# Optimization experiments

Hardware: AMD Instinct MI355X
Metric: run time of the kernel (lower is better)

Reference implementation:

```python
import jax, jax.numpy as jnp
import numpy as np

PI = float(np.pi)


def _layernorm(x, g, b, eps=1e-5):
    mu = jnp.mean(x, axis=-1, keepdims=True)
    var = jnp.var(x, axis=-1, keepdims=True)
    return (x - mu) * jax.lax.rsqrt(var + eps) * g + b


def setup_inputs() -> dict:
    key = jax.random.key(0)
    B, L, D, P = 4, 2048, 256, 32
    ks = jax.random.split(key, 16)

    def lin_w(k, fi, fo):
        return (jax.random.normal(k, (fi, fo), dtype=jnp.float32) / np.sqrt(fi)).astype(jnp.float32)

    inp = {
        'x': jax.random.normal(ks[0], (B, L, D), dtype=jnp.float32),
        'pos_phases': jax.random.normal(ks[1], (L, P), dtype=jnp.float32) * PI,
        'w_mem1v': lin_w(ks[2], D, P), 'b_mem1v': jnp.zeros((P,), jnp.float32),
        'w_mem1o': lin_w(ks[3], P, D), 'b_mem1o': jnp.zeros((D,), jnp.float32),
        'w_off': lin_w(ks[4], D + P, P), 'b_off': jnp.zeros((P,), jnp.float32),
        'w_key': lin_w(ks[5], D, P), 'b_key': jnp.zeros((P,), jnp.float32),
        'w_val': lin_w(ks[6], D, D), 'b_val': jnp.zeros((D,), jnp.float32),
        'w_sk1': lin_w(ks[7], 2 * D, D), 'b_sk1': jnp.zeros((D,), jnp.float32),
        'w_sk2': lin_w(ks[8], D, P), 'b_sk2': jnp.zeros((P,), jnp.float32),
        'w_gate': lin_w(ks[9], D, 1), 'b_gate': jnp.zeros((1,), jnp.float32),
        'ln_g': jnp.ones((D,), jnp.float32), 'ln_b': jnp.zeros((D,), jnp.float32),
        'w_out': lin_w(ks[10], D, D), 'b_out': jnp.zeros((D,), jnp.float32),
    }
    return inp


def reference(x, pos_phases, w_mem1v, b_mem1v, w_mem1o, b_mem1o, w_off, b_off,
              w_key, b_key, w_val, b_val, w_sk1, b_sk1, w_sk2, b_sk2,
              w_gate, b_gate, ln_g, ln_b, w_out, b_out):
    B, L, D = x.shape
    P = pos_phases.shape[-1]

    pos_cos = jnp.cos(pos_phases)  # [L,P]
    pos_sin = jnp.sin(pos_phases)

    # Memory 1: flat [B,L,P] phasor cumulative memory
    v1 = x @ w_mem1v + b_mem1v                       # [B,L,P]
    mem1_cos = jnp.cumsum(pos_cos[None] * v1, axis=1)
    mem1_sin = jnp.cumsum(pos_sin[None] * v1, axis=1)

    offset_input = jnp.concatenate([x, jnp.broadcast_to(pos_phases[None], (B, L, P))], axis=-1)
    offset = jnp.tanh(offset_input @ w_off + b_off) * PI
    oc, os = jnp.cos(offset), jnp.sin(offset)
    query_cos = pos_cos[None] * oc - pos_sin[None] * os
    query_sin = pos_sin[None] * oc + pos_cos[None] * os
    pos_ret = (mem1_cos * query_cos + mem1_sin * query_sin) / np.sqrt(P)
    pos_out = pos_ret @ w_mem1o + b_mem1o            # [B,L,D]

    # Memory 2: full [B,L,P,D] phasor KV cumulative memory
    key_phases = jnp.tanh(x @ w_key + b_key) * PI    # [B,L,P]
    key_cos, key_sin = jnp.cos(key_phases), jnp.sin(key_phases)
    values = x @ w_val + b_val                       # [B,L,D]
    store_gate = jax.nn.sigmoid(x @ w_gate + b_gate) # [B,L,1]

    positions = jnp.arange(1, L + 1, dtype=x.dtype)[None, :, None]
    context_avg = jnp.cumsum(x, axis=1) / positions
    h = jax.nn.gelu(jnp.concatenate([x, context_avg], axis=-1) @ w_sk1 + b_sk1, approximate=False)
    storage_phases = jnp.tanh(h @ w_sk2 + b_sk2) * PI  # [B,L,P]

    gated_v = values * store_gate                    # [B,L,D]
    kv_mem_cos = jnp.cumsum(jnp.cos(storage_phases)[..., None] * gated_v[:, :, None, :], axis=1)  # [B,L,P,D]
    kv_mem_sin = jnp.cumsum(jnp.sin(storage_phases)[..., None] * gated_v[:, :, None, :], axis=1)

    gate_cumsum = jnp.clip(jnp.cumsum(store_gate, axis=1), 1.0, None)  # [B,L,1]
    kv_retrieved = jnp.einsum('blpd,blp->bld', kv_mem_cos, key_cos) + \
                   jnp.einsum('blpd,blp->bld', kv_mem_sin, key_sin)
    kv_retrieved = kv_retrieved / (jnp.sqrt(gate_cumsum) * np.sqrt(P))

    combined = pos_out + kv_retrieved
    return x + _layernorm(combined, ln_g, ln_b) @ w_out + b_out
```

## Files before the change

### kernel.cpp

```cpp
#include <hip/hip_runtime.h>
#include <hip/hip_bf16.h>

constexpr int B_ = 4;
constexpr int L_ = 2048;
constexpr int D_ = 256;
constexpr int P_ = 32;
constexpr int CL = 32;
constexpr int NC = L_ / CL;

#define PI_F 3.14159265358979323846f
#define INV_SQRT_P 0.17677669529663687f

typedef __attribute__((ext_vector_type(8))) short short8_t;
typedef __attribute__((ext_vector_type(4))) float floatx4;

static __device__ inline short f2bf(float f) {
  unsigned int u;
  __builtin_memcpy(&u, &f, 4);
  unsigned int r = (u + 0x7fffu + ((u >> 16) & 1u)) >> 16;
  return (short)r;
}
static __device__ inline float bf2f(short s) {
  unsigned int u = ((unsigned int)(unsigned short)s) << 16;
  float f;
  __builtin_memcpy(&f, &u, 4);
  return f;
}

__global__ void wprep(const float* __restrict__ x, const float* __restrict__ pos,
                      const float* __restrict__ w_val, const float* __restrict__ w_mem1v,
                      const float* __restrict__ w_off, const float* __restrict__ b_off,
                      const float* __restrict__ w_key, const float* __restrict__ w_gate,
                      const float* __restrict__ w_sk1, const float* __restrict__ w_out,
                      const float* __restrict__ w_sk2, const float* __restrict__ w_mem1o,
                      short* __restrict__ WA, short* __restrict__ W1,
                      short* __restrict__ WO, short* __restrict__ W2T,
                      short* __restrict__ W1OT,
                      short* __restrict__ xbf, float* __restrict__ poff,
                      float* __restrict__ ctxsum) {
  int blk = blockIdx.x, tid = threadIdx.x;
  if (blk < 384) {
    int idx = blk * 256 + tid;
    int n = idx >> 8, k = idx & 255;
    float v;
    if (n < 256) v = w_val[k * 256 + n];
    else if (n < 288) v = w_mem1v[k * 32 + (n - 256)];
    else if (n < 320) v = w_off[k * 32 + (n - 288)];
    else if (n < 352) v = w_key[k * 32 + (n - 320)];
    else if (n == 352) v = w_gate[k];
    else v = 0.f;
    WA[idx] = f2bf(v);
  } else if (blk < 896) {
    int idx = (blk - 384) * 256 + tid;
    int n = idx >> 9, k = idx & 511;
    W1[idx] = f2bf(w_sk1[k * 256 + n]);
  } else if (blk < 1152) {
    int idx = (blk - 896) * 256 + tid;
    int n = idx >> 8, k = idx & 255;
    WO[idx] = f2bf(w_out[k * 256 + n]);
  } else if (blk < 1184) {
    int idx = (blk - 1152) * 256 + tid;
    int p = idx >> 8, k = idx & 255;
    W2T[idx] = f2bf(w_sk2[k * 32 + p]);
  } else if (blk < 1216) {
    int idx = (blk - 1184) * 256 + tid;
    int d = idx >> 5, p = idx & 31;
    W1OT[idx] = f2bf(w_mem1o[p * 256 + d]);
  } else if (blk < 3264) {
    int idx = ((blk - 1216) * 256 + tid) * 4;
    float4 v = *(const float4*)&x[idx];
    short4 o;
    o.x = f2bf(v.x); o.y = f2bf(v.y); o.z = f2bf(v.z); o.w = f2bf(v.w);
    *(short4*)&xbf[idx] = o;
  } else if (blk < 3520) {
    int idx = (blk - 3264) * 256 + tid;
    int l = idx >> 5, p = idx & 31;
    float a = b_off[p];
#pragma unroll 8
    for (int j = 0; j < 32; ++j) a += pos[l * 32 + j] * w_off[(256 + j) * 32 + p];
    poff[idx] = a;
  } else {
    int c2 = blk - 3520;
    int b = c2 >> 6, ch = c2 & 63;
    int xb = (b * L_ + ch * 32) * 256 + tid;
    float s = 0.f;
#pragma unroll 8
    for (int i = 0; i < 32; ++i) s += x[xb + i * 256];
    ctxsum[c2 * 256 + tid] = s;
  }
}

__global__ __launch_bounds__(384, 3) void gemmA3(const short* __restrict__ xbf,
                                                 const short* __restrict__ WA,
                                                 const float* __restrict__ pos,
                                                 const float* __restrict__ poff,
                                                 const float* __restrict__ b_mem1v,
                                                 const float* __restrict__ b_key,
                                                 const float* __restrict__ b_gate,
                                                 const float* __restrict__ b_val,
                                                 float* __restrict__ m1cT,
                                                 float* __restrict__ m1sT,
                                                 float* __restrict__ qc,
                                                 float* __restrict__ qs,
                                                 short* __restrict__ K2bf,
                                                 short* __restrict__ gvT,
                                                 float* __restrict__ sg) {
  __shared__ float YL[16][132];
  __shared__ float gsh[16];
  int tid = threadIdx.x;
  int lane = tid & 63, w = tid >> 6;
  int ml = lane & 15, quad = lane >> 4, kq = quad * 8;
  int bc = blockIdx.x;
  int bc32 = bc >> 1, half = bc & 1;
  int tok0 = bc * 16;
  floatx4 acc[4] = {};
  const short* A0p = &xbf[(tok0 + ml) * 256 + kq];
  const short* Bp = &WA[(w * 64 + ml) * 256 + kq];
#pragma unroll
  for (int ks = 0; ks < 8; ++ks) {
    short8_t a0 = *(const short8_t*)(A0p + ks * 32);
#pragma unroll
    for (int nt = 0; nt < 4; ++nt) {
      short8_t b = *(const short8_t*)(Bp + nt * 16 * 256 + ks * 32);
      acc[nt] = __builtin_amdgcn_mfma_f32_16x16x32_bf16(a0, b, acc[nt], 0, 0, 0);
    }
  }
  if (w >= 4) {
#pragma unroll
    for (int nt = 0; nt < 4; ++nt) {
      int col = (w - 4) * 64 + nt * 16 + ml;
#pragma unroll
      for (int r = 0; r < 4; ++r)
        YL[quad * 4 + r][col] = acc[nt][r];
    }
  }
  __syncthreads();
  if (tid < 256) {
#pragma unroll
    for (int it = 0; it < 2; ++it) {
      int idx = it * 256 + tid;
      int t = idx >> 5, p = idx & 31;
      int tok = tok0 + t, l = tok & (L_ - 1);
      int b = tok >> 11;
      float v1 = YL[t][p] + b_mem1v[p];
      float ph = pos[l * 32 + p];
      float pc = cosf(ph), ps = sinf(ph);
      int idxT = (b * 32 + p) * L_ + l;
      m1cT[idxT] = pc * v1;
      m1sT[idxT] = ps * v1;
      float off = tanhf(YL[t][32 + p] + poff[l * 32 + p]) * PI_F;
      float oc = cosf(off), os = sinf(off);
      int gidx = tok * 32 + p;
      qc[gidx] = pc * oc - ps * os;
      qs[gidx] = ps * oc + pc * os;
      float kp = tanhf(YL[t][64 + p] + b_key[p]) * PI_F;
      K2bf[tok * 64 + p] = f2bf(cosf(kp));
      K2bf[tok * 64 + 32 + p] = f2bf(sinf(kp));
      if (p == 0) {
        float g = 1.f / (1.f + expf(-(YL[t][96] + b_gate[0])));
        sg[tok] = g;
        gsh[t] = g;
      }
    }
  }
  __syncthreads();
  if (w < 4) {
#pragma unroll
    for (int nt = 0; nt < 4; ++nt) {
      int d = w * 64 + nt * 16 + ml;
      float bv = b_val[d];
      int t0 = quad * 4;
      short4 o;
      o.x = f2bf((acc[nt][0] + bv) * gsh[t0 + 0]);
      o.y = f2bf((acc[nt][1] + bv) * gsh[t0 + 1]);
      o.z = f2bf((acc[nt][2] + bv) * gsh[t0 + 2]);
      o.w = f2bf((acc[nt][3] + bv) * gsh[t0 + 3]);
      *(short4*)&gvT[(bc32 * 256 + d) * 32 + half * 16 + t0] = o;
    }
  }
}

__global__ void scan_all(float* __restrict__ m1cT, float* __restrict__ m1sT,
                         float* __restrict__ sg, const float* __restrict__ x,
                         const float* __restrict__ ctxsum, short* __restrict__ ctxbf) {
  int blk = blockIdx.x;
  int tid = threadIdx.x;
  if (blk >= 260) {
    int c2 = blk - 260;
    int b = c2 >> 6, ch = c2 & 63;
    float run = 0.f;
    int sb = b * 64 * 256 + tid;
    int c = 0;
    for (; c + 8 <= ch; c += 8) {
      float t0 = ctxsum[sb + (c + 0) * 256];
      float t1 = ctxsum[sb + (c + 1) * 256];
      float t2 = ctxsum[sb + (c + 2) * 256];
      float t3 = ctxsum[sb + (c + 3) * 256];
      float t4 = ctxsum[sb + (c + 4) * 256];
      float t5 = ctxsum[sb + (c + 5) * 256];
      float t6 = ctxsum[sb + (c + 6) * 256];
      float t7 = ctxsum[sb + (c + 7) * 256];
      run += ((t0 + t1) + (t2 + t3)) + ((t4 + t5) + (t6 + t7));
    }
    for (; c < ch; ++c) run += ctxsum[sb + c * 256];
    int xb = (b * L_ + ch * 32) * 256 + tid;
#pragma unroll 8
    for (int i = 0; i < 32; ++i) {
      run += x[xb + i * 256];
      int l = ch * 32 + i;
      ctxbf[xb + i * 256] = f2bf(run / (float)(l + 1));
    }
    return;
  }
  int lane = tid & 63, wid = tid >> 6;
  __shared__ float wsum[4];
  float carry = 0.f;
  float* arr;
  int base;
  if (blk < 256) {
    arr = (blk < 128) ? m1cT : m1sT;
    base = (blk & 127) * L_;
  } else {
    arr = sg;
    base = (blk - 256) * L_;
  }
  float v[8];
#pragma unroll
  for (int i = 0; i < 8; ++i) v[i] = arr[base + i * 256 + tid];
#pragma unroll
  for (int i = 0; i < 8; ++i) {
    float vv = v[i];
#pragma unroll
    for (int off = 1; off < 64; off <<= 1) {
      float n = __shfl_up(vv, off, 64);
      if (lane >= off) vv += n;
    }
    if (lane == 63) wsum[wid] = vv;
    __syncthreads();
    float add = carry;
    for (int w = 0; w < wid; ++w) add += wsum[w];
    arr[base + i * 256 + tid] = vv + add;
    carry += wsum[0] + wsum[1] + wsum[2] + wsum[3];
    __syncthreads();
  }
}

union __align__(16) CDMem {
  short As[32][520];
  struct { short HS[32][280]; short SPL[64][40]; } h;
};
__global__ __launch_bounds__(512, 4) void gemmCD(const short* __restrict__ xbf,
                                                 const short* __restrict__ ctxbf,
                                                 const short* __restrict__ W1,
                                                 const float* __restrict__ b_sk1,
                                                 const short* __restrict__ W2T,
                                                 const float* __restrict__ b_sk2,
                                                 const short* __restrict__ gvT,
                                                 short* __restrict__ SPbf,
                                                 short* __restrict__ UT) {
  __shared__ CDMem sm;
  int tid = threadIdx.x;
  int bc = blockIdx.x;
  int tok0 = bc * 32;
  int lane = tid & 63, w = tid >> 6;
  int ml = lane & 15, quad = lane >> 4, kq = quad * 8;
#pragma unroll
  for (int pass = 0; pass < 4; ++pass) {
    int idx = pass * 512 + tid;
    int row = idx >> 6, c8 = idx & 63;
    int col = c8 * 8;
    const short* src = (col < 256) ? &xbf[(tok0 + row) * 256 + col]
                                   : &ctxbf[(tok0 + row) * 256 + col - 256];
    *(short8_t*)&sm.As[row][col] = *(const short8_t*)src;
  }
  __syncthreads();
  int n0w = w * 32;
  floatx4 acc[2][2] = {};
#pragma unroll
  for (int kt = 0; kt < 16; ++kt) {
    short8_t a0 = *(short8_t*)&sm.As[ml][kt * 32 + kq];
    short8_t a1 = *(short8_t*)&sm.As[16 + ml][kt * 32 + kq];
    short8_t b0 = *(const short8_t*)&W1[(n0w + ml) * 512 + kt * 32 + kq];
    short8_t b1 = *(const short8_t*)&W1[(n0w + 16 + ml) * 512 + kt * 32 + kq];
    acc[0][0] = __builtin_amdgcn_mfma_f32_16x16x32_bf16(a0, b0, acc[0][0], 0, 0, 0);
    acc[0][1] = __builtin_amdgcn_mfma_f32_16x16x32_bf16(a0, b1, acc[0][1], 0, 0, 0);
    acc[1][0] = __builtin_amdgcn_mfma_f32_16x16x32_bf16(a1, b0, acc[1][0], 0, 0, 0);
    acc[1][1] = __builtin_amdgcn_mfma_f32_16x16x32_bf16(a1, b1, acc[1][1], 0, 0, 0);
  }
  short hv[2][2][4];
#pragma unroll
  for (int nt = 0; nt < 2; ++nt) {
    float bv = b_sk1[n0w + nt * 16 + ml];
#pragma unroll
    for (int mt = 0; mt < 2; ++mt)
#pragma unroll
      for (int r = 0; r < 4; ++r) {
        float v = acc[mt][nt][r] + bv;
        float g = 0.5f * v * (1.f + erff(v * 0.70710678118654752f));
        hv[mt][nt][r] = f2bf(g);
      }
  }
  __syncthreads();
#pragma unroll
  for (int mt = 0; mt < 2; ++mt)
#pragma unroll
    for (int nt = 0; nt < 2; ++nt)
#pragma unroll
      for (int r = 0; r < 4; ++r)
        sm.h.HS[mt * 16 + quad * 4 + r][n0w + nt * 16 + ml] = hv[mt][nt][r];
  __syncthreads();
  if (w < 4) {
    int th = w & 1, ph = w >> 1;
    floatx4 pacc = {};
#pragma unroll
    for (int s = 0; s < 8; ++s) {
      short8_t a = *(short8_t*)&sm.h.HS[th * 16 + ml][s * 32 + kq];
      short8_t b0 = *(const short8_t*)&W2T[(ph * 16 + ml) * 256 + s * 32 + kq];
      pacc = __builtin_amdgcn_mfma_f32_16x16x32_bf16(a, b0, pacc, 0, 0, 0);
    }
    int p = ph * 16 + ml;
    float bs = b_sk2[p];
#pragma unroll
    for (int r = 0; r < 4; ++r) {
      int tl = th * 16 + quad * 4 + r;
      int tok = tok0 + tl;
      float sp = tanhf(pacc[r] + bs) * PI_F;
      short c = f2bf(cosf(sp)), s2 = f2bf(sinf(sp));
      sm.h.SPL[p][tl] = c;
      sm.h.SPL[32 + p][tl] = s2;
      SPbf[tok * 64 + p] = c;
      SPbf[tok * 64 + 32 + p] = s2;
    }
  }
  __syncthreads();
  short8_t a[4];
#pragma unroll
  for (int mt = 0; mt < 4; ++mt) a[mt] = *(short8_t*)&sm.h.SPL[mt * 16 + ml][kq];
  floatx4 acc3[4][2] = {};
#pragma unroll
  for (int nt = 0; nt < 2; ++nt) {
    int d = w * 32 + nt * 16 + ml;
    short8_t b = *(const short8_t*)&gvT[(bc * 256 + d) * 32 + kq];
#pragma unroll
    for (int mt = 0; mt < 4; ++mt)
      acc3[mt][nt] = __builtin_amdgcn_mfma_f32_16x16x32_bf16(a[mt], b, acc3[mt][nt], 0, 0, 0);
  }
#pragma unroll
  for (int mt = 0; mt < 4; ++mt)
#pragma unroll
    for (int nt = 0; nt < 2; ++nt) {
      int d = w * 32 + nt * 16 + ml;
      short4 o;
      o.x = f2bf(acc3[mt][nt][0]);
      o.y = f2bf(acc3[mt][nt][1]);
      o.z = f2bf(acc3[mt][nt][2]);
      o.w = f2bf(acc3[mt][nt][3]);
      *(short4*)&UT[(bc * 256 + d) * 64 + mt * 16 + quad * 4] = o;
    }
}

__global__ void kernelE(short* __restrict__ UT) {
  int t = blockIdx.x * 256 + threadIdx.x;
  int pi = t >> 1, half = t & 1;
  int q = pi & 63;
  int d = (pi >> 6) & 255;
  int b = pi >> 14;
  const int cs = 256 * 64;
  int base = ((b * NC) * 256 + d) * 64 + q + half * 32 * cs;
  short v[32];
#pragma unroll
  for (int c = 0; c < 32; ++c) v[c] = UT[base + c * cs];
  float tot = 0.f;
#pragma unroll
  for (int c = 0; c < 32; ++c) tot += bf2f(v[c]);
  float other = __shfl_xor(tot, 1, 64);
  float run = half ? other : 0.f;
#pragma unroll
  for (int c = 0; c < 32; ++c) {
    UT[base + c * cs] = f2bf(run);
    run += bf2f(v[c]);
  }
}

struct __align__(16) FGMem {
  short SL[32][40];
  short PR[32][40];
  float CMB[32][260];
  short CBN[32][280];
  float LG[256], LB[256];
  float scl[32], mu_s[32], rs_s[32];
};
__global__ __launch_bounds__(512, 4) void fgOut(const short* __restrict__ UT,
                                                const short* __restrict__ SPbf,
                                                const short* __restrict__ K2bf,
                                                const short* __restrict__ gvT,
                                                const float* __restrict__ sgc,
                                                const float* __restrict__ m1cT,
                                                const float* __restrict__ m1sT,
                                                const float* __restrict__ qc,
                                                const float* __restrict__ qs,
                                                const short* __restrict__ W1OT,
                                                const float* __restrict__ b_mem1o,
                                                const float* __restrict__ ln_g,
                                                const float* __restrict__ ln_b,
                                                const short* __restrict__ WO,
                                                const float* __restrict__ b_out,
                                                const float* __restrict__ x,
                                                float* __restrict__ out) {
  __shared__ FGMem sm;
  int tid5 = threadIdx.x;
  int bc = blockIdx.x;
  int lbase = bc * CL;
  int bb = bc >> 6, lloc = (bc & 63) * 32;
  if (tid5 < 32) sm.scl[tid5] = rsqrtf(fmaxf(sgc[lbase + tid5], 1.f)) * INV_SQRT_P;
  if (tid5 >= 256 && tid5 < 512) {
    int d = tid5 - 256;
    sm.LG[d] = ln_g[d];
    sm.LB[d] = ln_b[d];
  }
#pragma unroll
  for (int it = 0; it < 2; ++it) {
    int i = it * 512 + tid5;
    int pp = i >> 5, t = i & 31;
    int gT = (bb * 32 + pp) * L_ + lloc + t;
    int g = (lbase + t) * 32 + pp;
    sm.PR[t][pp] = f2bf((m1cT[gT] * qc[g] + m1sT[gT] * qs[g]) * INV_SQRT_P);
  }
  int lane = tid5 & 63, w = tid5 >> 6;
  int ml = lane & 15, quad = lane >> 4, kq = quad * 8;
  int d0 = w * 32;
  floatx4 acc[2][2] = {};
  short8_t ka0 = *(const short8_t*)&K2bf[(lbase + ml) * 64 + kq];
  short8_t ka1 = *(const short8_t*)&K2bf[(lbase + 16 + ml) * 64 + kq];
  short8_t kb0 = *(const short8_t*)&K2bf[(lbase + ml) * 64 + 32 + kq];
  short8_t kb1 = *(const short8_t*)&K2bf[(lbase + 16 + ml) * 64 + 32 + kq];
#pragma unroll
  for (int nt = 0; nt < 2; ++nt) {
    short8_t b = *(const short8_t*)&UT[(bc * 256 + d0 + nt * 16 + ml) * 64 + kq];
    acc[0][nt] = __builtin_amdgcn_mfma_f32_16x16x32_bf16(ka0, b, acc[0][nt], 0, 0, 0);
    acc[1][nt] = __builtin_amdgcn_mfma_f32_16x16x32_bf16(ka1, b, acc[1][nt], 0, 0, 0);
  }
  if (w == 0) {
    floatx4 sacc[2][2] = {};
#pragma unroll
    for (int ks2 = 0; ks2 < 2; ++ks2) {
      short8_t a0 = (ks2 == 0) ? ka0 : kb0;
      short8_t a1 = (ks2 == 0) ? ka1 : kb1;
      short8_t b0 = *(const short8_t*)&SPbf[(lbase + ml) * 64 + ks2 * 32 + kq];
      short8_t b1 = *(const short8_t*)&SPbf[(lbase + 16 + ml) * 64 + ks2 * 32 + kq];
      sacc[0][0] = __builtin_amdgcn_mfma_f32_16x16x32_bf16(a0, b0, sacc[0][0], 0, 0, 0);
      sacc[0][1] = __builtin_amdgcn_mfma_f32_16x16x32_bf16(a0, b1, sacc[0][1], 0, 0, 0);
      sacc[1][0] = __builtin_amdgcn_mfma_f32_16x16x32_bf16(a1, b0, sacc[1][0], 0, 0, 0);
      sacc[1][1] = __builtin_amdgcn_mfma_f32_16x16x32_bf16(a1, b1, sacc[1][1], 0, 0, 0);
    }
#pragma unroll
    for (int mt = 0; mt < 2; ++mt)
#pragma unroll
      for (int nt = 0; nt < 2; ++nt)
#pragma unroll
        for (int r = 0; r < 4; ++r) {
          int trow = mt * 16 + quad * 4 + r;
          int scol = nt * 16 + ml;
          float v = (scol <= trow) ? sacc[mt][nt][r] : 0.f;
          sm.SL[trow][scol] = f2bf(v);
        }
  }
  __syncthreads();
#pragma unroll
  for (int nt = 0; nt < 2; ++nt) {
    short8_t b = *(const short8_t*)&UT[(bc * 256 + d0 + nt * 16 + ml) * 64 + 32 + kq];
    acc[0][nt] = __builtin_amdgcn_mfma_f32_16x16x32_bf16(kb0, b, acc[0][nt], 0, 0, 0);
    acc[1][nt] = __builtin_amdgcn_mfma_f32_16x16x32_bf16(kb1, b, acc[1][nt], 0, 0, 0);
  }
  {
    short8_t a0 = *(short8_t*)&sm.SL[ml][kq];
    short8_t a1 = *(short8_t*)&sm.SL[16 + ml][kq];
#pragma unroll
    for (int nt = 0; nt < 2; ++nt) {
      short8_t b = *(const short8_t*)&gvT[(bc * 256 + d0 + nt * 16 + ml) * 32 + kq];
      acc[0][nt] = __builtin_amdgcn_mfma_f32_16x16x32_bf16(a0, b, acc[0][nt], 0, 0, 0);
      acc[1][nt] = __builtin_amdgcn_mfma_f32_16x16x32_bf16(a1, b, acc[1][nt], 0, 0, 0);
    }
  }
  floatx4 macc[2][2] = {};
  {
    short8_t a0 = *(short8_t*)&sm.PR[ml][kq];
    short8_t a1 = *(short8_t*)&sm.PR[16 + ml][kq];
#pragma unroll
    for (int nt = 0; nt < 2; ++nt) {
      short8_t b = *(const short8_t*)&W1OT[(d0 + nt * 16 + ml) * 32 + kq];
      macc[0][nt] = __builtin_amdgcn_mfma_f32_16x16x32_bf16(a0, b, macc[0][nt], 0, 0, 0);
      macc[1][nt] = __builtin_amdgcn_mfma_f32_16x16x32_bf16(a1, b, macc[1][nt], 0, 0, 0);
    }
  }
#pragma unroll
  for (int mt = 0; mt < 2; ++mt)
#pragma unroll
    for (int nt = 0; nt < 2; ++nt) {
      int d = d0 + nt * 16 + ml;
      float bm = b_mem1o[d];
#pragma unroll
      for (int r = 0; r < 4; ++r) {
        int t = mt * 16 + quad * 4 + r;
        sm.CMB[t][d] = acc[mt][nt][r] * sm.scl[t] + macc[mt][nt][r] + bm;
      }
    }
  __syncthreads();
  {
    int t = tid5 >> 4, g = tid5 & 15;
    float s = 0.f, s2 = 0.f;
#pragma unroll
    for (int j = 0; j < 16; ++j) {
      float v = sm.CMB[t][g + j * 16];
      s += v;
      s2 += v * v;
    }
#pragma unroll
    for (int m = 1; m < 16; m <<= 1) {
      s += __shfl_xor(s, m, 64);
      s2 += __shfl_xor(s2, m, 64);
    }
    if (g == 0) {
      float mu = s / (float)D_;
      float var = s2 / (float)D_ - mu * mu;
      sm.mu_s[t] = mu;
      sm.rs_s[t] = rsqrtf(var + 1e-5f);
    }
  }
  __syncthreads();
#pragma unroll
  for (int it = 0; it < 16; ++it) {
    int i = it * 512 + tid5;
    int t = i >> 8, d = i & 255;
    sm.CBN[t][d] = f2bf((sm.CMB[t][d] - sm.mu_s[t]) * sm.rs_s[t] * sm.LG[d] + sm.LB[d]);
  }
  __syncthreads();
  floatx4 acc2[2][2] = {};
#pragma unroll
  for (int kt = 0; kt < 8; ++kt) {
    short8_t a0 = *(short8_t*)&sm.CBN[ml][kt * 32 + kq];
    short8_t a1 = *(short8_t*)&sm.CBN[16 + ml][kt * 32 + kq];
#pragma unroll
    for (int nt = 0; nt < 2; ++nt) {
      short8_t b = *(const short8_t*)&WO[(d0 + nt * 16 + ml) * 256 + kt * 32 + kq];
      acc2[0][nt] = __builtin_amdgcn_mfma_f32_16x16x32_bf16(a0, b, acc2[0][nt], 0, 0, 0);
      acc2[1][nt] = __builtin_amdgcn_mfma_f32_16x16x32_bf16(a1, b, acc2[1][nt], 0, 0, 0);
    }
  }
#pragma unroll
  for (int nt = 0; nt < 2; ++nt) {
    int n = d0 + nt * 16 + ml;
    float bv = b_out[n];
#pragma unroll
    for (int mt = 0; mt < 2; ++mt)
#pragma unroll
      for (int r = 0; r < 4; ++r) {
        int tok = lbase + mt * 16 + quad * 4 + r;
        out[tok * 256 + n] = x[tok * 256 + n] + acc2[mt][nt][r] + bv;
      }
  }
}

extern "C" void kernel_launch(void* const* d_in, const int* in_sizes, int n_in,
                              void* d_out, int out_size, void* d_ws, size_t ws_size,
                              hipStream_t stream) {
  const float* x = (const float*)d_in[0];
  const float* pos = (const float*)d_in[1];
  const float* w_mem1v = (const float*)d_in[2];
  const float* b_mem1v = (const float*)d_in[3];
  const float* w_mem1o = (const float*)d_in[4];
  const float* b_mem1o = (const float*)d_in[5];
  const float* w_off = (const float*)d_in[6];
  const float* b_off = (const float*)d_in[7];
  const float* w_key = (const float*)d_in[8];
  const float* b_key = (const float*)d_in[9];
  const float* w_val = (const float*)d_in[10];
  const float* b_val = (const float*)d_in[11];
  const float* w_sk1 = (const float*)d_in[12];
  const float* b_sk1 = (const float*)d_in[13];
  const float* w_sk2 = (const float*)d_in[14];
  const float* b_sk2 = (const float*)d_in[15];
  const float* w_gate = (const float*)d_in[16];
  const float* b_gate = (const float*)d_in[17];
  const float* ln_g = (const float*)d_in[18];
  const float* ln_b = (const float*)d_in[19];
  const float* w_out = (const float*)d_in[20];
  const float* b_out = (const float*)d_in[21];
  float* out = (float*)d_out;
  float* ws = (float*)d_ws;

  const int BLP = B_ * L_ * P_;
  const int BLD = B_ * L_ * D_;
  float* m1cT = ws;
  float* m1sT = m1cT + BLP;
  float* qc = m1sT + BLP;
  float* qs = qc + BLP;
  float* sg = qs + BLP;
  float* poff = sg + B_ * L_;
  float* ctxsum = poff + L_ * P_;
  short* UT = (short*)(ctxsum + B_ * 64 * 256);
  short* xbf = UT + (size_t)B_ * NC * 256 * 64;
  short* ctxbf = xbf + BLD;
  short* hs = ctxbf + BLD;
  short* gvT = hs + BLD;
  short* K2bf = gvT + BLD;
  short* SPbf = K2bf + B_ * L_ * 64;
  short* WA = SPbf + B_ * L_ * 64;
  short* W1 = WA + 384 * 256;
  short* WO = W1 + 256 * 512;
  short* W2T = WO + 256 * 256;
  short* W1OT = W2T + 32 * 256;

  wprep<<<3776, 256, 0, stream>>>(x, pos, w_val, w_mem1v, w_off, b_off, w_key, w_gate,
                                  w_sk1, w_out, w_sk2, w_mem1o, WA, W1, WO, W2T, W1OT,
                                  xbf, poff, ctxsum);
  gemmA3<<<512, 384, 0, stream>>>(xbf, WA, pos, poff, b_mem1v, b_key, b_gate, b_val,
                                  m1cT, m1sT, qc, qs, K2bf, gvT, sg);
  scan_all<<<516, 256, 0, stream>>>(m1cT, m1sT, sg, x, ctxsum, ctxbf);
  gemmCD<<<256, 512, 0, stream>>>(xbf, ctxbf, W1, b_sk1, W2T, b_sk2, gvT, SPbf, UT);
  kernelE<<<512, 256, 0, stream>>>(UT);
  fgOut<<<256, 512, 0, stream>>>(UT, SPbf, K2bf, gvT, sg, m1cT, m1sT, qc, qs,
                                 W1OT, b_mem1o, ln_g, ln_b, WO, b_out, x, out);
}
```

Baseline: 172.3 us.

## Fuse context-average computation into gemmCD and merge bf16 cast with chunk sums

Removes the ctxbf intermediate by computing the running context average directly into gemmCD's shared-memory A tile from x and the per-chunk sums. It also merges the x-to-bf16 conversion with the chunk-sum pass in wprep so x is read once there. The scan kernel is restructured so each wave scans a contiguous 512-element segment with a single barrier, and it is moved after kernelE. In fgOut, the PR tile build now runs on waves 1-7 alongside wave 0's MFMA work. Together these cut kernel launches work, global traffic and barriers, at the cost of gemmCD rereading x and recomputing chunk prefixes per block.

```diff
diff --git a/kernel.cpp b/kernel.cpp
--- a/kernel.cpp
+++ b/kernel.cpp
@@ -38,6 +38,7 @@
                       short* __restrict__ W1OT,
                       short* __restrict__ xbf, float* __restrict__ poff,
                       float* __restrict__ ctxsum) {
+  __shared__ float2 psum[2][128];
   int blk = blockIdx.x, tid = threadIdx.x;
   if (blk < 384) {
     int idx = blk * 256 + tid;
@@ -66,27 +67,39 @@
     int idx = (blk - 1184) * 256 + tid;
     int d = idx >> 5, p = idx & 31;
     W1OT[idx] = f2bf(w_mem1o[p * 256 + d]);
-  } else if (blk < 3264) {
-    int idx = ((blk - 1216) * 256 + tid) * 4;
-    float4 v = *(const float4*)&x[idx];
-    short4 o;
-    o.x = f2bf(v.x); o.y = f2bf(v.y); o.z = f2bf(v.z); o.w = f2bf(v.w);
-    *(short4*)&xbf[idx] = o;
-  } else if (blk < 3520) {
-    int idx = (blk - 3264) * 256 + tid;
+  } else if (blk < 1472) {
+    int idx = (blk - 1216) * 256 + tid;
     int l = idx >> 5, p = idx & 31;
     float a = b_off[p];
 #pragma unroll 8
     for (int j = 0; j < 32; ++j) a += pos[l * 32 + j] * w_off[(256 + j) * 32 + p];
     poff[idx] = a;
   } else {
-    int c2 = blk - 3520;
+    int c2 = blk - 1472;
     int b = c2 >> 6, ch = c2 & 63;
-    int xb = (b * L_ + ch * 32) * 256 + tid;
-    float s = 0.f;
-#pragma unroll 8
-    for (int i = 0; i < 32; ++i) s += x[xb + i * 256];
-    ctxsum[c2 * 256 + tid] = s;
+    int d2 = (tid & 127) * 2, h = tid >> 7;
+    int tokb = b * L_ + ch * 32 + h * 16;
+    float2 xv[16];
+#pragma unroll
+    for (int i = 0; i < 16; ++i)
+      xv[i] = *(const float2*)&x[(tokb + i) * 256 + d2];
+    float2 s = {0.f, 0.f};
+#pragma unroll
+    for (int i = 0; i < 16; ++i) { s.x += xv[i].x; s.y += xv[i].y; }
+#pragma unroll
+    for (int i = 0; i < 16; ++i) {
+      short2 o;
+      o.x = f2bf(xv[i].x);
+      o.y = f2bf(xv[i].y);
+      *(short2*)&xbf[(tokb + i) * 256 + d2] = o;
+    }
+    psum[h][tid & 127] = s;
+    __syncthreads();
+    if (h == 0) {
+      float2 o = psum[1][tid & 127];
+      float2 tot = {s.x + o.x, s.y + o.y};
+      *(float2*)&ctxsum[c2 * 256 + d2] = tot;
+    }
   }
 }
 
@@ -181,15 +194,78 @@
 }
 
 __global__ void scan_all(float* __restrict__ m1cT, float* __restrict__ m1sT,
-                         float* __restrict__ sg, const float* __restrict__ x,
-                         const float* __restrict__ ctxsum, short* __restrict__ ctxbf) {
+                         float* __restrict__ sg) {
+  __shared__ float wsum[4];
   int blk = blockIdx.x;
   int tid = threadIdx.x;
-  if (blk >= 260) {
-    int c2 = blk - 260;
-    int b = c2 >> 6, ch = c2 & 63;
-    float run = 0.f;
-    int sb = b * 64 * 256 + tid;
+  int lane = tid & 63, w = tid >> 6;
+  float* arr;
+  int base;
+  if (blk < 256) {
+    arr = (blk < 128) ? m1cT : m1sT;
+    base = (blk & 127) * L_;
+  } else {
+    arr = sg;
+    base = (blk - 256) * L_;
+  }
+  int sbase = base + w * 512;
+  float v[8];
+#pragma unroll
+  for (int i = 0; i < 8; ++i) v[i] = arr[sbase + i * 64 + lane];
+  float carry = 0.f;
+#pragma unroll
+  for (int i = 0; i < 8; ++i) {
+    float vv = v[i];
+#pragma unroll
+    for (int off = 1; off < 64; off <<= 1) {
+      float n = __shfl_up(vv, off, 64);
+      if (lane >= off) vv += n;
+    }
+    vv += carry;
+    v[i] = vv;
+    carry = __shfl(vv, 63, 64);
+  }
+  if (lane == 0) wsum[w] = carry;
+  __syncthreads();
+  float off = 0.f;
+  for (int ww = 0; ww < w; ++ww) off += wsum[ww];
+#pragma unroll
+  for (int i = 0; i < 8; ++i) arr[sbase + i * 64 + lane] = v[i] + off;
+}
+
+union __align__(16) CDMem {
+  short As[32][520];
+  struct { short HS[32][280]; short SPL[64][40]; } h;
+};
+__global__ __launch_bounds__(512, 4) void gemmCD(const short* __restrict__ xbf,
+                                                 const float* __restrict__ x,
+                                                 const float* __restrict__ ctxsum,
+                                                 const short* __restrict__ W1,
+                                                 const float* __restrict__ b_sk1,
+                                                 const short* __restrict__ W2T,
+                                                 const float* __restrict__ b_sk2,
+                                                 const short* __restrict__ gvT,
+                                                 short* __restrict__ SPbf,
+                                                 short* __restrict__ UT) {
+  __shared__ CDMem sm;
+  __shared__ float stmp[256];
+  int tid = threadIdx.x;
+  int bc = blockIdx.x;
+  int tok0 = bc * 32;
+  int bI = bc >> 6, ch = bc & 63;
+  int lane = tid & 63, w = tid >> 6;
+  int ml = lane & 15, quad = lane >> 4, kq = quad * 8;
+#pragma unroll
+  for (int pass = 0; pass < 2; ++pass) {
+    int idx = pass * 512 + tid;
+    int row = idx >> 5, c8 = idx & 31;
+    *(short8_t*)&sm.As[row][c8 * 8] =
+        *(const short8_t*)&xbf[(tok0 + row) * 256 + c8 * 8];
+  }
+  {
+    int d = tid & 255, h = tid >> 8;
+    float cp = 0.f;
+    int sb = bI * 64 * 256 + d;
     int c = 0;
     for (; c + 8 <= ch; c += 8) {
       float t0 = ctxsum[sb + (c + 0) * 256];
@@ -200,78 +276,25 @@
       float t5 = ctxsum[sb + (c + 5) * 256];
       float t6 = ctxsum[sb + (c + 6) * 256];
       float t7 = ctxsum[sb + (c + 7) * 256];
-      run += ((t0 + t1) + (t2 + t3)) + ((t4 + t5) + (t6 + t7));
-    }
-    for (; c < ch; ++c) run += ctxsum[sb + c * 256];
-    int xb = (b * L_ + ch * 32) * 256 + tid;
-#pragma unroll 8
-    for (int i = 0; i < 32; ++i) {
-      run += x[xb + i * 256];
-      int l = ch * 32 + i;
-      ctxbf[xb + i * 256] = f2bf(run / (float)(l + 1));
-    }
-    return;
-  }
-  int lane = tid & 63, wid = tid >> 6;
-  __shared__ float wsum[4];
-  float carry = 0.f;
-  float* arr;
-  int base;
-  if (blk < 256) {
-    arr = (blk < 128) ? m1cT : m1sT;
-    base = (blk & 127) * L_;
-  } else {
-    arr = sg;
-    base = (blk - 256) * L_;
-  }
-  float v[8];
-#pragma unroll
-  for (int i = 0; i < 8; ++i) v[i] = arr[base + i * 256 + tid];
-#pragma unroll
-  for (int i = 0; i < 8; ++i) {
-    float vv = v[i];
-#pragma unroll
-    for (int off = 1; off < 64; off <<= 1) {
-      float n = __shfl_up(vv, off, 64);
-      if (lane >= off) vv += n;
-    }
-    if (lane == 63) wsum[wid] = vv;
+      cp += ((t0 + t1) + (t2 + t3)) + ((t4 + t5) + (t6 + t7));
+    }
+    for (; c < ch; ++c) cp += ctxsum[sb + c * 256];
+    float xv[16];
+    int xb = (tok0 + h * 16) * 256 + d;
+#pragma unroll
+    for (int i = 0; i < 16; ++i) xv[i] = x[xb + i * 256];
+    float p = 0.f;
+#pragma unroll
+    for (int i = 0; i < 16; ++i) p += xv[i];
+    if (h == 0) stmp[d] = p;
     __syncthreads();
-    float add = carry;
-    for (int w = 0; w < wid; ++w) add += wsum[w];
-    arr[base + i * 256 + tid] = vv + add;
-    carry += wsum[0] + wsum[1] + wsum[2] + wsum[3];
-    __syncthreads();
-  }
-}
-
-union __align__(16) CDMem {
-  short As[32][520];
-  struct { short HS[32][280]; short SPL[64][40]; } h;
-};
-__global__ __launch_bounds__(512, 4) void gemmCD(const short* __restrict__ xbf,
-                                                 const short* __restrict__ ctxbf,
-                                                 const short* __restrict__ W1,
-                                                 const float* __restrict__ b_sk1,
-                                                 const short* __restrict__ W2T,
-                                                 const float* __restrict__ b_sk2,
-                                                 const short* __restrict__ gvT,
-                                                 short* __restrict__ SPbf,
-                                                 short* __restrict__ UT) {
-  __shared__ CDMem sm;
-  int tid = threadIdx.x;
-  int bc = blockIdx.x;
-  int tok0 = bc * 32;
-  int lane = tid & 63, w = tid >> 6;
-  int ml = lane & 15, quad = lane >> 4, kq = quad * 8;
-#pragma unroll
-  for (int pass = 0; pass < 4; ++pass) {
-    int idx = pass * 512 + tid;
-    int row = idx >> 6, c8 = idx & 63;
-    int col = c8 * 8;
-    const short* src = (col < 256) ? &xbf[(tok0 + row) * 256 + col]
-                                   : &ctxbf[(tok0 + row) * 256 + col - 256];
-    *(short8_t*)&sm.As[row][col] = *(const short8_t*)src;
+    float run = cp + (h ? stmp[d] : 0.f);
+    int l0 = ch * 32 + h * 16;
+#pragma unroll
+    for (int i = 0; i < 16; ++i) {
+      run += xv[i];
+      sm.As[h * 16 + i][256 + d] = f2bf(run / (float)(l0 + i + 1));
+    }
   }
   __syncthreads();
   int n0w = w * 32;
@@ -412,34 +435,19 @@
   int bc = blockIdx.x;
   int lbase = bc * CL;
   int bb = bc >> 6, lloc = (bc & 63) * 32;
+  int lane = tid5 & 63, w = tid5 >> 6;
+  int ml = lane & 15, quad = lane >> 4, kq = quad * 8;
+  int d0 = w * 32;
   if (tid5 < 32) sm.scl[tid5] = rsqrtf(fmaxf(sgc[lbase + tid5], 1.f)) * INV_SQRT_P;
-  if (tid5 >= 256 && tid5 < 512) {
+  if (tid5 >= 256) {
     int d = tid5 - 256;
     sm.LG[d] = ln_g[d];
     sm.LB[d] = ln_b[d];
   }
-#pragma unroll
-  for (int it = 0; it < 2; ++it) {
-    int i = it * 512 + tid5;
-    int pp = i >> 5, t = i & 31;
-    int gT = (bb * 32 + pp) * L_ + lloc + t;
-    int g = (lbase + t) * 32 + pp;
-    sm.PR[t][pp] = f2bf((m1cT[gT] * qc[g] + m1sT[gT] * qs[g]) * INV_SQRT_P);
-  }
-  int lane = tid5 & 63, w = tid5 >> 6;
-  int ml = lane & 15, quad = lane >> 4, kq = quad * 8;
-  int d0 = w * 32;
-  floatx4 acc[2][2] = {};
   short8_t ka0 = *(const short8_t*)&K2bf[(lbase + ml) * 64 + kq];
   short8_t ka1 = *(const short8_t*)&K2bf[(lbase + 16 + ml) * 64 + kq];
   short8_t kb0 = *(const short8_t*)&K2bf[(lbase + ml) * 64 + 32 + kq];
   short8_t kb1 = *(const short8_t*)&K2bf[(lbase + 16 + ml) * 64 + 32 + kq];
-#pragma unroll
-  for (int nt = 0; nt < 2; ++nt) {
-    short8_t b = *(const short8_t*)&UT[(bc * 256 + d0 + nt * 16 + ml) * 64 + kq];
-    acc[0][nt] = __builtin_amdgcn_mfma_f32_16x16x32_bf16(ka0, b, acc[0][nt], 0, 0, 0);
-    acc[1][nt] = __builtin_amdgcn_mfma_f32_16x16x32_bf16(ka1, b, acc[1][nt], 0, 0, 0);
-  }
   if (w == 0) {
     floatx4 sacc[2][2] = {};
 #pragma unroll
@@ -464,13 +472,25 @@
           float v = (scol <= trow) ? sacc[mt][nt][r] : 0.f;
           sm.SL[trow][scol] = f2bf(v);
         }
-  }
-  __syncthreads();
+  } else {
+    int t7 = tid5 - 64;
+    for (int i = t7; i < 1024; i += 448) {
+      int pp = i >> 5, t = i & 31;
+      int gT = (bb * 32 + pp) * L_ + lloc + t;
+      int g = (lbase + t) * 32 + pp;
+      sm.PR[t][pp] = f2bf((m1cT[gT] * qc[g] + m1sT[gT] * qs[g]) * INV_SQRT_P);
+    }
+  }
+  __syncthreads();
+  floatx4 acc[2][2] = {};
 #pragma unroll
   for (int nt = 0; nt < 2; ++nt) {
-    short8_t b = *(const short8_t*)&UT[(bc * 256 + d0 + nt * 16 + ml) * 64 + 32 + kq];
-    acc[0][nt] = __builtin_amdgcn_mfma_f32_16x16x32_bf16(kb0, b, acc[0][nt], 0, 0, 0);
-    acc[1][nt] = __builtin_amdgcn_mfma_f32_16x16x32_bf16(kb1, b, acc[1][nt], 0, 0, 0);
+    short8_t b0 = *(const short8_t*)&UT[(bc * 256 + d0 + nt * 16 + ml) * 64 + kq];
+    short8_t b1 = *(const short8_t*)&UT[(bc * 256 + d0 + nt * 16 + ml) * 64 + 32 + kq];
+    acc[0][nt] = __builtin_amdgcn_mfma_f32_16x16x32_bf16(ka0, b0, acc[0][nt], 0, 0, 0);
+    acc[1][nt] = __builtin_amdgcn_mfma_f32_16x16x32_bf16(ka1, b0, acc[1][nt], 0, 0, 0);
+    acc[0][nt] = __builtin_amdgcn_mfma_f32_16x16x32_bf16(kb0, b1, acc[0][nt], 0, 0, 0);
+    acc[1][nt] = __builtin_amdgcn_mfma_f32_16x16x32_bf16(kb1, b1, acc[1][nt], 0, 0, 0);
   }
   {
     short8_t a0 = *(short8_t*)&sm.SL[ml][kq];
@@ -611,14 +631,14 @@
   short* W2T = WO + 256 * 256;
   short* W1OT = W2T + 32 * 256;
 
-  wprep<<<3776, 256, 0, stream>>>(x, pos, w_val, w_mem1v, w_off, b_off, w_key, w_gate,
+  wprep<<<1728, 256, 0, stream>>>(x, pos, w_val, w_mem1v, w_off, b_off, w_key, w_gate,
                                   w_sk1, w_out, w_sk2, w_mem1o, WA, W1, WO, W2T, W1OT,
                                   xbf, poff, ctxsum);
   gemmA3<<<512, 384, 0, stream>>>(xbf, WA, pos, poff, b_mem1v, b_key, b_gate, b_val,
                                   m1cT, m1sT, qc, qs, K2bf, gvT, sg);
-  scan_all<<<516, 256, 0, stream>>>(m1cT, m1sT, sg, x, ctxsum, ctxbf);
-  gemmCD<<<256, 512, 0, stream>>>(xbf, ctxbf, W1, b_sk1, W2T, b_sk2, gvT, SPbf, UT);
+  gemmCD<<<256, 512, 0, stream>>>(xbf, x, ctxsum, W1, b_sk1, W2T, b_sk2, gvT, SPbf, UT);
   kernelE<<<512, 256, 0, stream>>>(UT);
+  scan_all<<<260, 256, 0, stream>>>(m1cT, m1sT, sg);
   fgOut<<<256, 512, 0, stream>>>(UT, SPbf, K2bf, gvT, sg, m1cT, m1sT, qc, qs,
                                  W1OT, b_mem1o, ln_g, ln_b, WO, b_out, x, out);
 }
```

Result: faster. 168.7 us (-2.1%).
